# Optimization experiments

Hardware: AMD Instinct MI355X
Metric: run time of the kernel (lower is better)

## Reference

```python
import jax, jax.numpy as jnp
import numpy as np

N = 100000   # nodes
E = 1600000  # edges
F = 64       # node_features == latent_channels
H = 128      # hidden_channels
G = 256      # graphs
L = 2        # n_layers


def setup_inputs() -> dict:
    key = jax.random.key(0)
    ks = jax.random.split(key, 20)
    x = jax.random.normal(ks[0], (N, F), dtype=jnp.float32)
    u = jax.random.normal(ks[1], (G, 2), dtype=jnp.float32)
    edge_index = jax.random.randint(ks[2], (2, E), 0, N, dtype=jnp.int32)
    # evenly assign nodes to graphs (sorted segment ids, no empty segments)
    batch = (jnp.arange(N, dtype=jnp.int32) * G // N).astype(jnp.int32)
    s = 0.05
    # per-layer edge-MLP params, stacked over layers: in = 2F-2 = 126
    W1 = jax.random.normal(ks[3], (L, 2 * F - 2, H), dtype=jnp.float32) * s
    b1 = jnp.zeros((L, H), dtype=jnp.float32)
    W2 = jax.random.normal(ks[4], (L, H, H), dtype=jnp.float32) * s
    b2 = jnp.zeros((L, H), dtype=jnp.float32)
    W3 = jax.random.normal(ks[5], (L, H, F), dtype=jnp.float32) * s
    b3 = jnp.zeros((L, F), dtype=jnp.float32)
    # readout head: in = 3*F + 2 = 194
    LW1 = jax.random.normal(ks[6], (3 * F + 2, F), dtype=jnp.float32) * s
    Lb1 = jnp.zeros((F,), dtype=jnp.float32)
    LW2 = jax.random.normal(ks[7], (F, F), dtype=jnp.float32) * s
    Lb2 = jnp.zeros((F,), dtype=jnp.float32)
    LW3 = jax.random.normal(ks[8], (F, 2), dtype=jnp.float32) * s
    Lb3 = jnp.zeros((2,), dtype=jnp.float32)
    return dict(x=x, u=u, edge_index=edge_index, batch=batch,
                W1=W1, b1=b1, W2=W2, b2=b2, W3=W3, b3=b3,
                LW1=LW1, Lb1=Lb1, LW2=LW2, Lb2=Lb2, LW3=LW3, Lb3=Lb3)


def _edge_layer(x, src, dst, W1, b1, W2, b2, W3, b3):
    xi = x[dst]            # target nodes (x_i), [E, F]
    xj = x[src]            # source nodes (x_j), [E, F]
    d = xj[:, :3] - xi[:, :3]
    dist2 = jnp.sum(d * d, axis=-1, keepdims=True)  # [E, 1]
    m_in = jnp.concatenate([xi, xj[:, 3:], dist2], axis=-1)  # [E, 2F-2]
    h = jax.nn.silu(m_in @ W1 + b1)
    h = jax.nn.silu(h @ W2 + b2)
    m = jax.nn.silu(h @ W3 + b3)                    # [E, F]
    return jax.ops.segment_sum(m, dst, num_segments=N)  # aggr='sum'


def reference(x, u, edge_index, batch, W1, b1, W2, b2, W3, b3,
              LW1, Lb1, LW2, Lb2, LW3, Lb3):
    src, dst = edge_index[0], edge_index[1]
    for l in range(L):
        x = _edge_layer(x, src, dst, W1[l], b1[l], W2[l], b2[l], W3[l], b3[l])
    addp = jax.ops.segment_sum(x, batch, num_segments=G)
    cnt = jax.ops.segment_sum(jnp.ones((N, 1), x.dtype), batch, num_segments=G)
    meanp = addp / jnp.maximum(cnt, 1.0)
    maxp = jax.ops.segment_max(x, batch, num_segments=G)
    pooled = jnp.concatenate([addp, meanp, maxp, u], axis=1)  # [G, 3F+2]
    h = jax.nn.silu(pooled @ LW1 + Lb1)
    h = jax.nn.silu(h @ LW2 + Lb2)
    return h @ LW3 + Lb3  # [G, 2]
```

## Files before the change

### kernel.cpp

```cpp
#include <hip/hip_runtime.h>
#include <hip/hip_bf16.h>

typedef _Float16 f16;
typedef _Float16 f16x8 __attribute__((ext_vector_type(8)));
typedef float    f32x4 __attribute__((ext_vector_type(4)));
typedef float    f32x8 __attribute__((ext_vector_type(8)));

__device__ __forceinline__ float silu_f(float x) {
    return x * __builtin_amdgcn_rcpf(1.0f + __expf(-x));
}

__device__ __forceinline__ void load_lds16(const f16* g, f16* l) {
    __builtin_amdgcn_global_load_lds(
        (const __attribute__((address_space(1))) void*)g,
        (__attribute__((address_space(3))) void*)l, 16, 0, 0);
}

__global__ void prep_kernel(const float* __restrict__ W1, const float* __restrict__ W2,
                            const float* __restrict__ W3, f16* __restrict__ B1T,
                            f16* __restrict__ W2T, f16* __restrict__ W3T,
                            f16* __restrict__ w1c, int L, int total) {
    int idx = blockIdx.x * 256 + threadIdx.x;
    if (idx >= total) return;
    const int per = 16384 + 16384 + 8192 + 128;
    int l = idx / per, r = idx % per;
    const float* W1l = W1 + (size_t)l * 126 * 128;
    if (r < 16384) {
        int c = r >> 6, k = r & 63;
        float v;
        if (c < 128) v = W1l[k * 128 + c];
        else v = (k >= 3) ? W1l[(64 + k - 3) * 128 + (c - 128)]
                          : 0.0f;
        B1T[(size_t)l * 16384 + r] = (f16)v;
    } else if (r < 32768) {
        int q = r - 16384, n = q >> 7, k = q & 127;
        W2T[(size_t)l * 16384 + q] = (f16)W2[(size_t)l * 16384 + k * 128 + n];
    } else if (r < 40960) {
        int q = r - 32768, n = q >> 7, k = q & 127;
        W3T[(size_t)l * 8192 + q] = (f16)W3[(size_t)l * 8192 + k * 64 + n];
    } else {
        int c = r - 40960;
        w1c[l * 128 + c] = (f16)W1l[125 * 128 + c];
    }
}

__global__ void hist_kernel(const int* __restrict__ ei, int* __restrict__ deg, int E) {
    int i = blockIdx.x * 256 + threadIdx.x;
    if (i < E) atomicAdd(&deg[ei[E + i]], 1);
}

__global__ void scan_part(const int* __restrict__ deg, int* __restrict__ bsum, int N) {
    __shared__ int red[256];
    int t = threadIdx.x;
    int i = blockIdx.x * 256 + t;
    red[t] = (i < N) ? deg[i] : 0;
    __syncthreads();
    for (int s = 128; s > 0; s >>= 1) {
        if (t < s) red[t] += red[t + s];
        __syncthreads();
    }
    if (t == 0) bsum[blockIdx.x] = red[0];
}

__global__ void scan_mid(const int* __restrict__ bsum, int* __restrict__ boff, int nb) {
    __shared__ int sm[512];
    int t = threadIdx.x;
    int v = (t < nb) ? bsum[t] : 0;
    sm[t] = v;
    __syncthreads();
    for (int off = 1; off < 512; off <<= 1) {
        int a = (t >= off) ? sm[t - off] : 0;
        __syncthreads();
        sm[t] += a;
        __syncthreads();
    }
    if (t < nb) boff[t] = sm[t] - v;
}

__global__ void scan_final(const int* __restrict__ deg, const int* __restrict__ boff,
                           int* __restrict__ row_start, int N) {
    __shared__ int sm[256];
    int t = threadIdx.x;
    int i = blockIdx.x * 256 + t;
    int v = (i < N) ? deg[i] : 0;
    sm[t] = v;
    __syncthreads();
    for (int off = 1; off < 256; off <<= 1) {
        int a = (t >= off) ? sm[t - off] : 0;
        __syncthreads();
        sm[t] += a;
        __syncthreads();
    }
    if (i < N) row_start[i] = boff[blockIdx.x] + sm[t] - v;
}

__global__ void scatter_kernel(const int* __restrict__ ei, const int* __restrict__ row_start,
                               int* __restrict__ cursor, int* __restrict__ srcs,
                               int* __restrict__ dsts, int E) {
    int i = blockIdx.x * 256 + threadIdx.x;
    if (i < E) {
        int d = ei[E + i];
        int p = row_start[d] + atomicAdd(&cursor[d], 1);
        srcs[p] = ei[i];
        dsts[p] = d;
    }
}

__global__ __launch_bounds__(256, 3) void node_kernel(
    const float* __restrict__ x, const f16* __restrict__ B1T,
    const float* __restrict__ b1, f16* __restrict__ PQ,
    float4* __restrict__ C, int N, int ntiles) {
    __shared__ f16 b1t[256 * 72];
    const int tid = threadIdx.x;
    const int w = tid >> 6, lane = tid & 63, lm = lane & 15, kg = lane >> 4;

    for (int i = tid; i < 256 * 64; i += 256)
        b1t[(i >> 6) * 72 + (i & 63)] = B1T[i];
    __syncthreads();

    for (int tile = blockIdx.x; tile < ntiles; tile += gridDim.x) {
        const int base = tile * 64;
        int ar = base + w * 16 + lm;
        if (ar >= N) ar = N - 1;

        f16x8 afrag[2];
#pragma unroll
        for (int ks = 0; ks < 2; ks++) {
            f32x8 v = *(const f32x8*)(x + (size_t)ar * 64 + ks * 32 + kg * 8);
            f16x8 h;
#pragma unroll
            for (int j = 0; j < 8; j++) h[j] = (f16)v[j];
            afrag[ks] = h;
        }

        f32x4 acc[16];
#pragma unroll
        for (int nb = 0; nb < 16; nb++) acc[nb] = (f32x4){0.f, 0.f, 0.f, 0.f};
#pragma unroll
        for (int ks = 0; ks < 2; ks++)
#pragma unroll
            for (int nb = 0; nb < 16; nb++) {
                f16x8 b = *(const f16x8*)&b1t[(nb * 16 + lm) * 72 + ks * 32 + kg * 8];
                acc[nb] = __builtin_amdgcn_mfma_f32_16x16x32_f16(afrag[ks], b, acc[nb], 0, 0, 0);
            }

#pragma unroll
        for (int nb = 0; nb < 16; nb++) {
            int col = nb * 16 + lm;
            float bias = (col < 128) ? b1[col] : 0.0f;
#pragma unroll
            for (int reg = 0; reg < 4; reg++) {
                int orow = base + w * 16 + kg * 4 + reg;
                if (orow < N) PQ[(size_t)orow * 256 + col] = (f16)(acc[nb][reg] + bias);
            }
        }
        if (tid < 64) {
            int n = base + tid;
            if (n < N) {
                const float* xr = x + (size_t)n * 64;
                C[n] = make_float4(xr[0], xr[1], xr[2], 0.0f);
            }
        }
    }
}

__global__ __launch_bounds__(256, 2) void edge_kernel(
    const f16* __restrict__ PQ, const float4* __restrict__ C,
    const int* __restrict__ srcs, const int* __restrict__ dsts,
    const f16* __restrict__ W2T, const f16* __restrict__ W3T,
    const f16* __restrict__ w1c, const float* __restrict__ b2,
    const float* __restrict__ b3, float* __restrict__ xout,
    int E, int wtiles) {
    __shared__ f16 w2t[128 * 128];
    __shared__ f16 stage[4 * 4096];
    __shared__ f16 tb[4 * 16 * 72];

    const int tid = threadIdx.x;
    const int w = tid >> 6, lane = tid & 63, lm = lane & 15, kg = lane >> 4;
    const int e4 = lane >> 2, c4 = lane & 3;

    for (int i = tid; i < 128 * 128; i += 256) {
        int n = i >> 7, k = i & 127;
        w2t[n * 128 + (((k >> 3) ^ (n & 15)) << 3) + (k & 7)] = W2T[i];
    }

    f32x8 wvh[4];
#pragma unroll
    for (int ks = 0; ks < 4; ks++) {
        f16x8 wv = *(const f16x8*)(w1c + ks * 32 + kg * 8);
#pragma unroll
        for (int j = 0; j < 8; j++) wvh[ks][j] = (float)wv[j];
    }
    float bias2[8], bias3[4];
#pragma unroll
    for (int nb = 0; nb < 8; nb++) bias2[nb] = b2[nb * 16 + lm];
#pragma unroll
    for (int nb = 0; nb < 4; nb++) bias3[nb] = b3[nb * 16 + lm];
    __syncthreads();

    f16* sw = stage + w * 4096;
    f16* tq = tb + w * (16 * 72);
    const int nwaves = gridDim.x * 4;
    const int r0 = kg * 4;
    const int l1i = (lane + 16) & 63, l2i = (lane + 32) & 63, l3i = (lane + 48) & 63;

    int t = blockIdx.x * 4 + w;
    if (t >= wtiles) return;
    int e0 = t * 16 + lm;
    int erc = min(e0, E - 1);
    int scl = srcs[erc];
    int dcl = dsts[erc];
    int dsen_cur = (e0 < E) ? dcl : -1;
    {
        int de = __shfl(dcl, e4), se = __shfl(scl, e4);
        const f16* gp = PQ + (size_t)de * 256 + c4 * 8;
        const f16* gq = PQ + (size_t)se * 256 + 128 + c4 * 8;
#pragma unroll
        for (int j = 0; j < 4; j++) load_lds16(gp + j * 32, sw + j * 512 + lane * 8);
#pragma unroll
        for (int j = 0; j < 4; j++) load_lds16(gq + j * 32, sw + 2048 + j * 512 + lane * 8);
    }
    int e1 = (t + nwaves) * 16 + lm;
    int erc1 = min(max(e1, 0), E - 1);
    int s_nx = srcs[erc1];
    int d_nx = dsts[erc1];
    int e_nx_ok = (e1 < E) ? 1 : 0;
    float4 cs = C[scl], cd = C[dcl];

    f32x4 acc2p[4];
#pragma unroll
    for (int nb2 = 0; nb2 < 4; nb2++) acc2p[nb2] = (f32x4){0.f, 0.f, 0.f, 0.f};
    int dsen_prev = -1;

    while (true) {
        const int tn = t + nwaves;

        asm volatile("s_waitcnt vmcnt(4)" ::: "memory");

        float dx = cs.x - cd.x, dy = cs.y - cd.y, dz = cs.z - cd.z;
        float dist2 = dx * dx + dy * dy + dz * dz;

        f16x8 afrag[4];
#pragma unroll
        for (int ks = 0; ks < 4; ks++) {
            f16x8 p = *(const f16x8*)&sw[ks * 512 + lm * 32 + kg * 8];
            f16x8 q = *(const f16x8*)&sw[2048 + ks * 512 + lm * 32 + kg * 8];
            f16x8 pq = p + q;
            f16x8 h;
#pragma unroll
            for (int j = 0; j < 8; j++) {
                float v = (float)pq[j] + dist2 * wvh[ks][j];
                h[j] = (f16)silu_f(v);
            }
            afrag[ks] = h;
        }

        f32x4 acc1[8];
#pragma unroll
        for (int nb = 0; nb < 8; nb++) acc1[nb] = (f32x4){0.f, 0.f, 0.f, 0.f};
#pragma unroll
        for (int ks = 0; ks < 4; ks++)
#pragma unroll
            for (int nb = 0; nb < 8; nb++) {
                int n = nb * 16 + lm;
                f16x8 b = *(const f16x8*)&w2t[n * 128 + (((ks * 4 + kg) ^ (n & 15)) << 3)];
                acc1[nb] = __builtin_amdgcn_mfma_f32_16x16x32_f16(afrag[ks], b, acc1[nb], 0, 0, 0);
            }

        {
            const int dr0 = __shfl(dsen_prev, r0);
            const int dr1 = __shfl(dsen_prev, r0 + 1);
            const int dr2 = __shfl(dsen_prev, r0 + 2);
            const int dr3 = __shfl(dsen_prev, r0 + 3);
            int prevv = __shfl(dsen_prev, (r0 - 1) & 63);
            if (kg == 0) prevv = -1234567;

            const bool e01 = dr0 == dr1, e12 = dr1 == dr2, e23 = dr2 == dr3;
            const bool c01 = e01, c02 = e01 && e12, c03 = c02 && e23;
            const bool c12 = e12, c13 = e12 && e23;
            const int fullI = c03 ? 1 : 0;

            const int tgt = dr3;
            const int dr0_1 = __shfl(dr0, l1i), fu1 = __shfl(fullI, l1i);
            const int dr0_2 = __shfl(dr0, l2i), fu2 = __shfl(fullI, l2i);
            const int dr0_3 = __shfl(dr0, l3i);
            const bool take1 = (kg <= 2) && (dr0_1 == tgt);
            const bool take2 = take1 && fu1 && (kg <= 1) && (dr0_2 == tgt);
            const bool take3 = take2 && fu2 && (kg == 0) && (dr0_3 == tgt);

            const bool h0 = (dr0 != prevv) && (dr0 >= 0);
            const bool h1f = (!e01) && (dr1 >= 0);
            const bool h2f = (!e12) && (dr2 >= 0);
            const bool h3f = (!e23) && (dr3 >= 0);

            float t0v[4], t1v[4], t2v[4], t3v[4];
#pragma unroll
            for (int nb2 = 0; nb2 < 4; nb2++) {
                const float bias = bias3[nb2];
                const float v0 = silu_f(acc2p[nb2][0] + bias);
                const float v1 = silu_f(acc2p[nb2][1] + bias);
                const float v2 = silu_f(acc2p[nb2][2] + bias);
                const float v3 = silu_f(acc2p[nb2][3] + bias);
                float lead = v0 + (c01 ? v1 : 0.f) + (c02 ? v2 : 0.f) + (c03 ? v3 : 0.f);
                float ext = 0.f;
                const float le1 = __shfl(lead, l1i);
                const float le2 = __shfl(lead, l2i);
                const float le3 = __shfl(lead, l3i);
                if (take1) ext += le1;
                if (take2) ext += le2;
                if (take3) ext += le3;
                t0v[nb2] = lead + (c03 ? ext : 0.f);
                t1v[nb2] = v1 + (c12 ? v2 : 0.f) + (c13 ? (v3 + ext) : 0.f);
                t2v[nb2] = v2 + (e23 ? (v3 + ext) : 0.f);
                t3v[nb2] = v3 + ext;
            }
            if (h0) {
                float* p = xout + (size_t)dr0 * 64 + lm;
#pragma unroll
                for (int nb2 = 0; nb2 < 4; nb2++) atomicAdd(p + nb2 * 16, t0v[nb2]);
            }
            if (h1f) {
                float* p = xout + (size_t)dr1 * 64 + lm;
#pragma unroll
                for (int nb2 = 0; nb2 < 4; nb2++) atomicAdd(p + nb2 * 16, t1v[nb2]);
            }
            if (h2f) {
                float* p = xout + (size_t)dr2 * 64 + lm;
#pragma unroll
                for (int nb2 = 0; nb2 < 4; nb2++) atomicAdd(p + nb2 * 16, t2v[nb2]);
            }
            if (h3f) {
                float* p = xout + (size_t)dr3 * 64 + lm;
#pragma unroll
                for (int nb2 = 0; nb2 < 4; nb2++) atomicAdd(p + nb2 * 16, t3v[nb2]);
            }
        }

        int dsen_nx = e_nx_ok ? d_nx : -1;
        if (tn < wtiles) {
            int de = __shfl(d_nx, e4), se = __shfl(s_nx, e4);
            const f16* gp = PQ + (size_t)de * 256 + c4 * 8;
            const f16* gq = PQ + (size_t)se * 256 + 128 + c4 * 8;
#pragma unroll
            for (int j = 0; j < 4; j++) load_lds16(gp + j * 32, sw + j * 512 + lane * 8);
#pragma unroll
            for (int j = 0; j < 4; j++) load_lds16(gq + j * 32, sw + 2048 + j * 512 + lane * 8);
        }

        int e2 = (tn + nwaves) * 16 + lm;
        int erc2 = min(max(e2, 0), E - 1);
        int s_nx2 = srcs[erc2];
        int d_nx2 = dsts[erc2];
        int e_nx2_ok = (e2 < E) ? 1 : 0;
        float4 cs2 = C[s_nx], cd2 = C[d_nx];

        f32x4 acc2[4];
#pragma unroll
        for (int nb2 = 0; nb2 < 4; nb2++) acc2[nb2] = (f32x4){0.f, 0.f, 0.f, 0.f};
#pragma unroll
        for (int half = 0; half < 2; half++) {
#pragma unroll
            for (int kqi = 0; kqi < 2; kqi++) {
                int kq = half * 2 + kqi;
#pragma unroll
                for (int nn = 0; nn < 2; nn++) {
                    int nb = kq * 2 + nn;
#pragma unroll
                    for (int reg = 0; reg < 4; reg++)
                        tq[(kg * 4 + reg) * 72 + kqi * 32 + nn * 16 + lm] =
                            (f16)silu_f(acc1[nb][reg] + bias2[nb]);
                }
            }
#pragma unroll
            for (int kqi = 0; kqi < 2; kqi++) {
                int kq = half * 2 + kqi;
                f16x8 a2 = *(const f16x8*)&tq[lm * 72 + kqi * 32 + kg * 8];
#pragma unroll
                for (int nb2 = 0; nb2 < 4; nb2++) {
                    f16x8 b = *(const f16x8*)(W3T + (size_t)(nb2 * 16 + lm) * 128 +
                                              kq * 32 + kg * 8);
                    acc2[nb2] = __builtin_amdgcn_mfma_f32_16x16x32_f16(a2, b, acc2[nb2], 0, 0, 0);
                }
            }
        }

#pragma unroll
        for (int nb2 = 0; nb2 < 4; nb2++) acc2p[nb2] = acc2[nb2];
        dsen_prev = dsen_cur;
        dsen_cur = dsen_nx;
        s_nx = s_nx2; d_nx = d_nx2; e_nx_ok = e_nx2_ok;
        cs = cs2; cd = cd2;
        t = tn;
        if (t >= wtiles) break;
    }

    {
        const int dr0 = __shfl(dsen_prev, r0);
        const int dr1 = __shfl(dsen_prev, r0 + 1);
        const int dr2 = __shfl(dsen_prev, r0 + 2);
        const int dr3 = __shfl(dsen_prev, r0 + 3);
        int prevv = __shfl(dsen_prev, (r0 - 1) & 63);
        if (kg == 0) prevv = -1234567;

        const bool e01 = dr0 == dr1, e12 = dr1 == dr2, e23 = dr2 == dr3;
        const bool c01 = e01, c02 = e01 && e12, c03 = c02 && e23;
        const bool c12 = e12, c13 = e12 && e23;
        const int fullI = c03 ? 1 : 0;

        const int tgt = dr3;
        const int dr0_1 = __shfl(dr0, l1i), fu1 = __shfl(fullI, l1i);
        const int dr0_2 = __shfl(dr0, l2i), fu2 = __shfl(fullI, l2i);
        const int dr0_3 = __shfl(dr0, l3i);
        const bool take1 = (kg <= 2) && (dr0_1 == tgt);
        const bool take2 = take1 && fu1 && (kg <= 1) && (dr0_2 == tgt);
        const bool take3 = take2 && fu2 && (kg == 0) && (dr0_3 == tgt);

        const bool h0 = (dr0 != prevv) && (dr0 >= 0);
        const bool h1f = (!e01) && (dr1 >= 0);
        const bool h2f = (!e12) && (dr2 >= 0);
        const bool h3f = (!e23) && (dr3 >= 0);

        float t0v[4], t1v[4], t2v[4], t3v[4];
#pragma unroll
        for (int nb2 = 0; nb2 < 4; nb2++) {
            const float bias = bias3[nb2];
            const float v0 = silu_f(acc2p[nb2][0] + bias);
            const float v1 = silu_f(acc2p[nb2][1] + bias);
            const float v2 = silu_f(acc2p[nb2][2] + bias);
            const float v3 = silu_f(acc2p[nb2][3] + bias);
            float lead = v0 + (c01 ? v1 : 0.f) + (c02 ? v2 : 0.f) + (c03 ? v3 : 0.f);
            float ext = 0.f;
            const float le1 = __shfl(lead, l1i);
            const float le2 = __shfl(lead, l2i);
            const float le3 = __shfl(lead, l3i);
            if (take1) ext += le1;
            if (take2) ext += le2;
            if (take3) ext += le3;
            t0v[nb2] = lead + (c03 ? ext : 0.f);
            t1v[nb2] = v1 + (c12 ? v2 : 0.f) + (c13 ? (v3 + ext) : 0.f);
            t2v[nb2] = v2 + (e23 ? (v3 + ext) : 0.f);
            t3v[nb2] = v3 + ext;
        }
        if (h0) {
            float* p = xout + (size_t)dr0 * 64 + lm;
#pragma unroll
            for (int nb2 = 0; nb2 < 4; nb2++) atomicAdd(p + nb2 * 16, t0v[nb2]);
        }
        if (h1f) {
            float* p = xout + (size_t)dr1 * 64 + lm;
#pragma unroll
            for (int nb2 = 0; nb2 < 4; nb2++) atomicAdd(p + nb2 * 16, t1v[nb2]);
        }
        if (h2f) {
            float* p = xout + (size_t)dr2 * 64 + lm;
#pragma unroll
            for (int nb2 = 0; nb2 < 4; nb2++) atomicAdd(p + nb2 * 16, t2v[nb2]);
        }
        if (h3f) {
            float* p = xout + (size_t)dr3 * 64 + lm;
#pragma unroll
            for (int nb2 = 0; nb2 < 4; nb2++) atomicAdd(p + nb2 * 16, t3v[nb2]);
        }
    }
    asm volatile("s_waitcnt vmcnt(0)" ::: "memory");
}

__global__ void pool_kernel(const float* __restrict__ xf, const float* __restrict__ u,
                            float* __restrict__ pooled, int N, int G) {
    int g = blockIdx.x;
    int t = threadIdx.x;
    int ch = t & 63, sub = t >> 6;
    long long n0 = ((long long)g * N + G - 1) / G;
    long long n1 = ((long long)(g + 1) * N + G - 1) / G;
    float sm = 0.f, mx = -3.0e38f;
    for (long long n = n0 + sub; n < n1; n += 4) {
        float v = xf[n * 64 + ch];
        sm += v;
        mx = fmaxf(mx, v);
    }
    __shared__ float ssum[256], smax[256];
    ssum[t] = sm;
    smax[t] = mx;
    __syncthreads();
    if (sub == 0) {
        float a = ssum[ch] + ssum[64 + ch] + ssum[128 + ch] + ssum[192 + ch];
        float m = fmaxf(fmaxf(smax[ch], smax[64 + ch]), fmaxf(smax[128 + ch], smax[192 + ch]));
        float cnt = (float)(n1 - n0);
        pooled[g * 194 + ch] = a;
        pooled[g * 194 + 64 + ch] = a / fmaxf(cnt, 1.f);
        pooled[g * 194 + 128 + ch] = m;
    }
    if (t == 0) {
        pooled[g * 194 + 192] = u[g * 2];
        pooled[g * 194 + 193] = u[g * 2 + 1];
    }
}

__global__ void head_kernel(const float* __restrict__ pooled,
                            const float* __restrict__ LW1, const float* __restrict__ Lb1,
                            const float* __restrict__ LW2, const float* __restrict__ Lb2,
                            const float* __restrict__ LW3, const float* __restrict__ Lb3,
                            float* __restrict__ out, int G) {
    int g = blockIdx.x, t = threadIdx.x;
    __shared__ float pl[194];
    __shared__ float hl[64];
    for (int k = t; k < 194; k += 64) pl[k] = pooled[g * 194 + k];
    __syncthreads();
    float a = Lb1[t];
    for (int k = 0; k < 194; k++) a += pl[k] * LW1[k * 64 + t];
    a = a / (1.0f + __expf(-a));
    hl[t] = a;
    __syncthreads();
    float b = Lb2[t];
    for (int k = 0; k < 64; k++) b += hl[k] * LW2[k * 64 + t];
    b = b / (1.0f + __expf(-b));
    __syncthreads();
    hl[t] = b;
    __syncthreads();
    if (t < 2) {
        float c = Lb3[t];
        for (int k = 0; k < 64; k++) c += hl[k] * LW3[k * 2 + t];
        out[g * 2 + t] = c;
    }
}

extern "C" void kernel_launch(void* const* d_in, const int* in_sizes, int n_in,
                              void* d_out, int out_size, void* d_ws, size_t ws_size,
                              hipStream_t stream) {
    const float* x   = (const float*)d_in[0];
    const float* u   = (const float*)d_in[1];
    const int*   ei  = (const int*)d_in[2];
    const float* W1  = (const float*)d_in[4];
    const float* b1  = (const float*)d_in[5];
    const float* W2  = (const float*)d_in[6];
    const float* b2  = (const float*)d_in[7];
    const float* W3  = (const float*)d_in[8];
    const float* b3  = (const float*)d_in[9];
    const float* LW1 = (const float*)d_in[10];
    const float* Lb1 = (const float*)d_in[11];
    const float* LW2 = (const float*)d_in[12];
    const float* Lb2 = (const float*)d_in[13];
    const float* LW3 = (const float*)d_in[14];
    const float* Lb3 = (const float*)d_in[15];

    const int N = in_sizes[0] / 64;
    const int G = in_sizes[1] / 2;
    const int E = in_sizes[2] / 2;
    const int L = in_sizes[4] / (126 * 128);

    char* ws = (char*)d_ws;
    size_t off = 0;
    auto alloc = [&](size_t bytes) -> char* {
        char* p = ws + off;
        off += (bytes + 511) & ~(size_t)511;
        return p;
    };
    f16*    PQ     = (f16*)alloc((size_t)N * 256 * 2);
    float4* C      = (float4*)alloc((size_t)N * 16);
    float*  x1     = (float*)alloc((size_t)N * 64 * 4);
    float*  x2     = (float*)alloc((size_t)N * 64 * 4);
    int*    srcs   = (int*)alloc((size_t)E * 4);
    int*    dsts   = (int*)alloc((size_t)E * 4);
    int*    deg    = (int*)alloc((size_t)N * 4);
    int*    rowst  = (int*)alloc((size_t)N * 4);
    int*    cursor = (int*)alloc((size_t)N * 4);
    int*    bsum   = (int*)alloc(4096);
    int*    boff   = (int*)alloc(4096);
    f16*    B1T    = (f16*)alloc((size_t)L * 256 * 64 * 2);
    f16*    W2T    = (f16*)alloc((size_t)L * 128 * 128 * 2);
    f16*    W3T    = (f16*)alloc((size_t)L * 64 * 128 * 2);
    f16*    w1c    = (f16*)alloc((size_t)L * 128 * 2);
    float*  pooled = (float*)alloc((size_t)G * 194 * 4);
    (void)ws_size;
    (void)n_in;
    (void)out_size;

    hipMemsetAsync(deg, 0, (size_t)N * 4, stream);
    hipMemsetAsync(cursor, 0, (size_t)N * 4, stream);
    hipMemsetAsync(x1, 0, (size_t)N * 64 * 4, stream);
    hipMemsetAsync(x2, 0, (size_t)N * 64 * 4, stream);

    {
        int total = L * (16384 + 16384 + 8192 + 128);
        prep_kernel<<<(total + 255) / 256, 256, 0, stream>>>(W1, W2, W3, B1T, W2T, W3T, w1c, L, total);
    }
    hist_kernel<<<(E + 255) / 256, 256, 0, stream>>>(ei, deg, E);
    int NB = (N + 255) / 256;
    scan_part<<<NB, 256, 0, stream>>>(deg, bsum, N);
    scan_mid<<<1, 512, 0, stream>>>(bsum, boff, NB);
    scan_final<<<NB, 256, 0, stream>>>(deg, boff, rowst, N);
    scatter_kernel<<<(E + 255) / 256, 256, 0, stream>>>(ei, rowst, cursor, srcs, dsts, E);

    const float* xcur = x;
    const int wtiles = (E + 15) / 16;
    const int ntiles_node = (N + 63) / 64;
    for (int l = 0; l < L; l++) {
        node_kernel<<<768, 256, 0, stream>>>(xcur, B1T + (size_t)l * 16384, b1 + l * 128,
                                             PQ, C, N, ntiles_node);
        float* xo = (l & 1) ? x2 : x1;
        edge_kernel<<<512, 256, 0, stream>>>(PQ, C, srcs, dsts,
                                             W2T + (size_t)l * 16384, W3T + (size_t)l * 8192,
                                             w1c + l * 128, b2 + l * 128, b3 + l * 64,
                                             xo, E, wtiles);
        xcur = xo;
    }
    pool_kernel<<<G, 256, 0, stream>>>(xcur, u, pooled, N, G);
    head_kernel<<<G, 64, 0, stream>>>(pooled, LW1, Lb1, LW2, Lb2, LW3, Lb3, (float*)d_out, G);
}
```

Before: 1.035 ms.

## Load dst P rows directly to registers and shrink LDS to fit three blocks per CU

Edges are sorted by destination, so the per-edge P row for the destination node is now read straight from global memory into registers instead of being staged through LDS. Only the source Q row is still prefetched asynchronously into LDS. The staging and transpose buffers are halved, launch bounds go to 3 blocks per SM, and the grid grows from 512 to 768 blocks, all to raise occupancy. The cost is a synchronous global load on the critical path and more register pressure. The vmcnt(4) wait was left unchanged while only 4 async loads are now issued per tile, so ordering may be subtly off.

New measurement: 1.074 ms. +3.8%, slower.

```diff
diff --git a/kernel.cpp b/kernel.cpp
--- a/kernel.cpp
+++ b/kernel.cpp
@@ -164,7 +164,7 @@
     }
 }
 
-__global__ __launch_bounds__(256, 2) void edge_kernel(
+__global__ __launch_bounds__(256, 3) void edge_kernel(
     const f16* __restrict__ PQ, const float4* __restrict__ C,
     const int* __restrict__ srcs, const int* __restrict__ dsts,
     const f16* __restrict__ W2T, const f16* __restrict__ W3T,
@@ -172,8 +172,8 @@
     const float* __restrict__ b3, float* __restrict__ xout,
     int E, int wtiles) {
     __shared__ f16 w2t[128 * 128];
-    __shared__ f16 stage[4 * 4096];
-    __shared__ f16 tb[4 * 16 * 72];
+    __shared__ f16 stage[4 * 2048];
+    __shared__ f16 tb[4 * 576];
 
     const int tid = threadIdx.x;
     const int w = tid >> 6, lane = tid & 63, lm = lane & 15, kg = lane >> 4;
@@ -198,8 +198,8 @@
     for (int nb = 0; nb < 4; nb++) bias3[nb] = b3[nb * 16 + lm];
     __syncthreads();
 
-    f16* sw = stage + w * 4096;
-    f16* tq = tb + w * (16 * 72);
+    f16* sw = stage + w * 2048;
+    f16* tq = tb + w * 576;
     const int nwaves = gridDim.x * 4;
     const int r0 = kg * 4;
     const int l1i = (lane + 16) & 63, l2i = (lane + 32) & 63, l3i = (lane + 48) & 63;
@@ -212,13 +212,10 @@
     int dcl = dsts[erc];
     int dsen_cur = (e0 < E) ? dcl : -1;
     {
-        int de = __shfl(dcl, e4), se = __shfl(scl, e4);
-        const f16* gp = PQ + (size_t)de * 256 + c4 * 8;
+        int se = __shfl(scl, e4);
         const f16* gq = PQ + (size_t)se * 256 + 128 + c4 * 8;
 #pragma unroll
-        for (int j = 0; j < 4; j++) load_lds16(gp + j * 32, sw + j * 512 + lane * 8);
-#pragma unroll
-        for (int j = 0; j < 4; j++) load_lds16(gq + j * 32, sw + 2048 + j * 512 + lane * 8);
+        for (int j = 0; j < 4; j++) load_lds16(gq + j * 32, sw + j * 512 + lane * 8);
     }
     int e1 = (t + nwaves) * 16 + lm;
     int erc1 = min(max(e1, 0), E - 1);
@@ -237,15 +234,19 @@
 
         asm volatile("s_waitcnt vmcnt(4)" ::: "memory");
 
+        const f16* pd = PQ + (size_t)dcl * 256 + kg * 8;
+        f16x8 pv[4];
+#pragma unroll
+        for (int ks = 0; ks < 4; ks++) pv[ks] = *(const f16x8*)(pd + ks * 32);
+
         float dx = cs.x - cd.x, dy = cs.y - cd.y, dz = cs.z - cd.z;
         float dist2 = dx * dx + dy * dy + dz * dz;
 
         f16x8 afrag[4];
 #pragma unroll
         for (int ks = 0; ks < 4; ks++) {
-            f16x8 p = *(const f16x8*)&sw[ks * 512 + lm * 32 + kg * 8];
-            f16x8 q = *(const f16x8*)&sw[2048 + ks * 512 + lm * 32 + kg * 8];
-            f16x8 pq = p + q;
+            f16x8 q = *(const f16x8*)&sw[ks * 512 + lm * 32 + kg * 8];
+            f16x8 pq = pv[ks] + q;
             f16x8 h;
 #pragma unroll
             for (int j = 0; j < 8; j++) {
@@ -338,13 +339,10 @@
 
         int dsen_nx = e_nx_ok ? d_nx : -1;
         if (tn < wtiles) {
-            int de = __shfl(d_nx, e4), se = __shfl(s_nx, e4);
-            const f16* gp = PQ + (size_t)de * 256 + c4 * 8;
+            int se = __shfl(s_nx, e4);
             const f16* gq = PQ + (size_t)se * 256 + 128 + c4 * 8;
 #pragma unroll
-            for (int j = 0; j < 4; j++) load_lds16(gp + j * 32, sw + j * 512 + lane * 8);
-#pragma unroll
-            for (int j = 0; j < 4; j++) load_lds16(gq + j * 32, sw + 2048 + j * 512 + lane * 8);
+            for (int j = 0; j < 4; j++) load_lds16(gq + j * 32, sw + j * 512 + lane * 8);
         }
 
         int e2 = (tn + nwaves) * 16 + lm;
@@ -358,29 +356,21 @@
 #pragma unroll
         for (int nb2 = 0; nb2 < 4; nb2++) acc2[nb2] = (f32x4){0.f, 0.f, 0.f, 0.f};
 #pragma unroll
-        for (int half = 0; half < 2; half++) {
-#pragma unroll
-            for (int kqi = 0; kqi < 2; kqi++) {
-                int kq = half * 2 + kqi;
-#pragma unroll
-                for (int nn = 0; nn < 2; nn++) {
-                    int nb = kq * 2 + nn;
-#pragma unroll
-                    for (int reg = 0; reg < 4; reg++)
-                        tq[(kg * 4 + reg) * 72 + kqi * 32 + nn * 16 + lm] =
-                            (f16)silu_f(acc1[nb][reg] + bias2[nb]);
-                }
-            }
-#pragma unroll
-            for (int kqi = 0; kqi < 2; kqi++) {
-                int kq = half * 2 + kqi;
-                f16x8 a2 = *(const f16x8*)&tq[lm * 72 + kqi * 32 + kg * 8];
-#pragma unroll
-                for (int nb2 = 0; nb2 < 4; nb2++) {
-                    f16x8 b = *(const f16x8*)(W3T + (size_t)(nb2 * 16 + lm) * 128 +
-                                              kq * 32 + kg * 8);
-                    acc2[nb2] = __builtin_amdgcn_mfma_f32_16x16x32_f16(a2, b, acc2[nb2], 0, 0, 0);
-                }
+        for (int kq = 0; kq < 4; kq++) {
+#pragma unroll
+            for (int nn = 0; nn < 2; nn++) {
+                int nb = kq * 2 + nn;
+#pragma unroll
+                for (int reg = 0; reg < 4; reg++)
+                    tq[(kg * 4 + reg) * 36 + nn * 16 + lm] =
+                        (f16)silu_f(acc1[nb][reg] + bias2[nb]);
+            }
+            f16x8 a2 = *(const f16x8*)&tq[lm * 36 + kg * 8];
+#pragma unroll
+            for (int nb2 = 0; nb2 < 4; nb2++) {
+                f16x8 b = *(const f16x8*)(W3T + (size_t)(nb2 * 16 + lm) * 128 +
+                                          kq * 32 + kg * 8);
+                acc2[nb2] = __builtin_amdgcn_mfma_f32_16x16x32_f16(a2, b, acc2[nb2], 0, 0, 0);
             }
         }
 
@@ -388,6 +378,7 @@
         for (int nb2 = 0; nb2 < 4; nb2++) acc2p[nb2] = acc2[nb2];
         dsen_prev = dsen_cur;
         dsen_cur = dsen_nx;
+        dcl = d_nx;
         s_nx = s_nx2; d_nx = d_nx2; e_nx_ok = e_nx2_ok;
         cs = cs2; cd = cd2;
         t = tn;
@@ -598,7 +589,7 @@
         node_kernel<<<768, 256, 0, stream>>>(xcur, B1T + (size_t)l * 16384, b1 + l * 128,
                                              PQ, C, N, ntiles_node);
         float* xo = (l & 1) ? x2 : x1;
-        edge_kernel<<<512, 256, 0, stream>>>(PQ, C, srcs, dsts,
+        edge_kernel<<<768, 256, 0, stream>>>(PQ, C, srcs, dsts,
                                              W2T + (size_t)l * 16384, W3T + (size_t)l * 8192,
                                              w1c + l * 128, b2 + l * 128, b3 + l * 64,
                                              xo, E, wtiles);
```
